# Performance work log

Hardware: AMD Instinct MI355X
Metric: run time of the kernel (lower is better)

The kernel has to match this reference:

```python
import jax, jax.numpy as jnp
import numpy as np

N, D, K = 16384, 256, 4096  # encoded vectors, embedding_dim, codebook_size


def setup_inputs() -> dict:
    key = jax.random.key(0)
    k_ze, k_cb = jax.random.split(key)
    ze = jax.random.normal(k_ze, (N, D), dtype=jnp.float32)
    codebook = jax.random.normal(k_cb, (K, D), dtype=jnp.float32)
    return {"ze": ze, "codebook": codebook}


def reference(ze, codebook):
    # Pairwise squared distances: ||ze||^2 + ||e||^2 - 2 ze e^T  -> [N, K]
    sq_norm = (
        jnp.sum(ze ** 2, axis=-1, keepdims=True)
        + jnp.sum(codebook ** 2, axis=1)
        - 2.0 * jnp.matmul(ze, codebook.T)
    )
    indices = jnp.argmin(sq_norm, axis=-1)            # [N]
    zq = jnp.take(codebook, indices, axis=0)          # [N, D] gather

    # VQ losses (stop-gradient mirrors .detach())
    vq_e_loss = jnp.mean((zq - jax.lax.stop_gradient(ze)) ** 2)
    vq_commit_loss = jnp.mean((jax.lax.stop_gradient(zq) - ze) ** 2)

    # perplexity: probs[i] = count_i / 10 (faithful to original, incl. /10)
    counts = jnp.zeros((K,), dtype=jnp.float32).at[indices].add(1.0)
    probs = counts / 10.0
    perplexity = jnp.exp(-jnp.sum(probs * jnp.log(probs + 1e-10)))

    return indices, zq, vq_e_loss, vq_commit_loss, perplexity
```

## Files before the change

### kernel.cpp

```cpp
#include <hip/hip_runtime.h>
#include <math.h>

#define N_TOT 16384
#define DIM   256
#define KCB   4096

typedef __attribute__((ext_vector_type(8)))  short s8v;
typedef __attribute__((ext_vector_type(16))) float f16v;

#define PK_OFF   32832
#define CBF_OFF  163904
#define WS_NEED  4358208ull
#define ZERO_W   36880

__device__ __forceinline__ void gload16(const void* g, void* l) {
  __builtin_amdgcn_global_load_lds(
      (const __attribute__((address_space(1))) unsigned int*)g,
      (__attribute__((address_space(3))) unsigned int*)l, 16, 0, 0);
}

__global__ __launch_bounds__(256)
void cb_prep_k(const float* __restrict__ cb, float* __restrict__ ws) {
  const int t = threadIdx.x, tile = blockIdx.x;
  for (int i = tile * 256 + t; i < ZERO_W; i += 128 * 256) ws[KCB + i] = 0.0f;

  const int col = t >> 3, j = t & 7;
  const int c0  = tile * 32;
  ushort* tb = (ushort*)((char*)ws + CBF_OFF) + (size_t)tile * 16384;
  const float* src = cb + (size_t)(c0 + col) * DIM;
  float s = 0.0f;
  #pragma unroll
  for (int ks = 0; ks < 16; ++ks) {
    #pragma unroll
    for (int kh = 0; kh < 2; ++kh) {
      float x = src[ks * 16 + kh * 8 + j];
      s += x * x;
      unsigned xb = __float_as_uint(x);
      unsigned hb = xb & 0xFFFF0000u;
      float lf = x - __uint_as_float(hb);
      tb[ks * 512 + kh * 256 + t]        = (ushort)(xb >> 16);
      tb[8192 + ks * 512 + kh * 256 + t] = (ushort)(__float_as_uint(lf) >> 16);
    }
  }
  s += __shfl_down(s, 4, 8);
  s += __shfl_down(s, 2, 8);
  s += __shfl_down(s, 1, 8);
  if (j == 0) ws[c0 + col] = s;
}

#define AP 260

__global__ __launch_bounds__(512, 2)
void vq_mfma_k(const float* __restrict__ ze, float* __restrict__ ws) {
  __shared__ __align__(16) char ldsU[66560];

  const int t    = threadIdx.x;
  const int lane = t & 63;
  const int w    = t >> 6;
  const int ln31 = lane & 31;
  const int hl   = lane >> 5;
  const int mb   = blockIdx.x >> 2;
  const int cq   = blockIdx.x & 3;
  const int m0   = mb * 256;

  const float* cbn = ws;
  unsigned long long* pk = (unsigned long long*)((char*)ws + PK_OFF);
  const char* cbF = (const char*)ws + CBF_OFF;

  s8v ah[16], al[16];
  float* Af = (float*)ldsU;
  for (int c = 0; c < 4; ++c) {
    __syncthreads();
    {
      int r  = t >> 3;
      int f0 = t & 7;
      const float* src = ze + (size_t)(m0 + c * 64 + r) * DIM;
      #pragma unroll
      for (int i = 0; i < 8; ++i) {
        int f = f0 + 8 * i;
        *(float4*)&Af[r * AP + f * 4] = *(const float4*)(src + f * 4);
      }
    }
    __syncthreads();
    if ((w >> 1) == c) {
      int rl = (w & 1) * 32 + ln31;
      #pragma unroll
      for (int ks = 0; ks < 16; ++ks) {
        float4 x0 = *(const float4*)&Af[rl * AP + ks * 16 + hl * 8];
        float4 x1 = *(const float4*)&Af[rl * AP + ks * 16 + hl * 8 + 4];
        float xs[8] = {x0.x, x0.y, x0.z, x0.w, x1.x, x1.y, x1.z, x1.w};
        #pragma unroll
        for (int j = 0; j < 8; ++j) {
          unsigned xb = __float_as_uint(xs[j]);
          unsigned hb = xb & 0xFFFF0000u;
          float lf = xs[j] - __uint_as_float(hb);
          ah[ks][j] = (short)(xb >> 16);
          al[ks][j] = (short)(__float_as_uint(lf) >> 16);
        }
      }
    }
  }
  __syncthreads();

  char* bufs0 = ldsU;
  char* bufs1 = ldsU + 32768;
  const char* qbase = cbF + (size_t)cq * 32 * 32768;

  {
    const char* g = qbase + (size_t)w * 4096 + (size_t)lane * 16;
    char* lp = bufs0 + w * 4096;
    #pragma unroll
    for (int ii = 0; ii < 4; ++ii) gload16(g + ii * 1024, lp + ii * 1024);
  }

  float best[16];
  int   bidx[16];
  #pragma unroll
  for (int r = 0; r < 16; ++r) { best[r] = -1e30f; bidx[r] = 0; }

  #pragma unroll 1
  for (int tt = 0; tt < 32; ++tt) {
    __syncthreads();
    if (tt + 1 < 32) {
      const char* g = qbase + (size_t)(tt + 1) * 32768 + (size_t)w * 4096 + (size_t)lane * 16;
      char* lp = ((tt + 1) & 1 ? bufs1 : bufs0) + w * 4096;
      #pragma unroll
      for (int ii = 0; ii < 4; ++ii) gload16(g + ii * 1024, lp + ii * 1024);
    }

    const int   c0      = cq * 1024 + tt * 32;
    const float half_cv = 0.5f * cbn[c0 + ln31];
    const char* bc      = (tt & 1) ? bufs1 : bufs0;

    f16v hh, xx;
    #pragma unroll
    for (int r = 0; r < 16; ++r) { hh[r] = 0.0f; xx[r] = 0.0f; }

    #pragma unroll
    for (int ks = 0; ks < 16; ++ks) {
      s8v bh = *(const s8v*)(bc + ks * 1024 + lane * 16);
      s8v bl = *(const s8v*)(bc + 16384 + ks * 1024 + lane * 16);
      hh = __builtin_amdgcn_mfma_f32_32x32x16_bf16(ah[ks], bh, hh, 0, 0, 0);
      xx = __builtin_amdgcn_mfma_f32_32x32x16_bf16(ah[ks], bl, xx, 0, 0, 0);
      xx = __builtin_amdgcn_mfma_f32_32x32x16_bf16(al[ks], bh, xx, 0, 0, 0);
    }

    #pragma unroll
    for (int r = 0; r < 16; ++r) {
      float s = hh[r] + xx[r] - half_cv;
      if (s > best[r]) { best[r] = s; bidx[r] = c0 + ln31; }
    }
  }

  #pragma unroll
  for (int r = 0; r < 16; ++r) {
    float s = best[r];
    int   c = bidx[r];
    #pragma unroll
    for (int mk = 1; mk < 32; mk <<= 1) {
      float os = __shfl_xor(s, mk, 64);
      int   oc = __shfl_xor(c, mk, 64);
      if (os > s || (os == s && oc < c)) { s = os; c = oc; }
    }
    if (ln31 == 0) {
      int row = m0 + w * 32 + (r & 3) + 8 * (r >> 2) + 4 * hl;
      unsigned u = __float_as_uint(s);
      unsigned enc = (u & 0x80000000u) ? ~u : (u | 0x80000000u);
      unsigned long long p = ((unsigned long long)enc << 32) | (unsigned)(KCB - 1 - c);
      atomicMax(&pk[row], p);
    }
  }
}

__global__ __launch_bounds__(256)
void gather_k(const float* __restrict__ ze, const float* __restrict__ cb,
              float* __restrict__ ws, float* __restrict__ out) {
  __shared__ int sIdx[64];
  const int t  = threadIdx.x;
  const int m0 = blockIdx.x * 64;
  float* counts   = ws + KCB;
  float* loss_sum = ws + 2 * KCB;
  const unsigned long long* pk = (const unsigned long long*)((const char*)ws + PK_OFF);

  if (t < 64) {
    unsigned long long p = pk[m0 + t];
    int col = KCB - 1 - (int)(unsigned)(p & 0xFFFFFFFFull);
    out[m0 + t] = (float)col;
    sIdx[t] = col;
    atomicAdd(&counts[col], 1.0f);
  }
  __syncthreads();

  float* out_zq = out + N_TOT;
  const int w = t >> 6, ln = t & 63;
  float lsum = 0.0f;
  #pragma unroll
  for (int p = 0; p < 16; ++p) {
    int r = w + 4 * p;
    float4 cvv = *(const float4*)(cb + (size_t)sIdx[r] * DIM + ln * 4);
    float4 zv  = *(const float4*)(ze + (size_t)(m0 + r) * DIM + ln * 4);
    *(float4*)(out_zq + (size_t)(m0 + r) * DIM + ln * 4) = cvv;
    float dx = cvv.x - zv.x, dy = cvv.y - zv.y, dz = cvv.z - zv.z, dw = cvv.w - zv.w;
    lsum += dx * dx + dy * dy + dz * dz + dw * dw;
  }
  #pragma unroll
  for (int off = 32; off > 0; off >>= 1) lsum += __shfl_down(lsum, off, 64);
  if (ln == 0) atomicAdd(loss_sum, lsum);
}

__global__ void zero_ws_k(float* __restrict__ ws, int nw) {
  int i = blockIdx.x * 256 + threadIdx.x;
  if (i < nw) ws[KCB + i] = 0.0f;
}

__global__ void cbnorm_k(const float* __restrict__ cb, float* __restrict__ ws) {
  int row  = blockIdx.x * 4 + (threadIdx.x >> 6);
  int lane = threadIdx.x & 63;
  float4 v = *(const float4*)(cb + (size_t)row * DIM + lane * 4);
  float s = v.x*v.x + v.y*v.y + v.z*v.z + v.w*v.w;
  #pragma unroll
  for (int off = 32; off > 0; off >>= 1) s += __shfl_down(s, off, 64);
  if (lane == 0) ws[row] = s;
}

#define FBM 32
#define FBN 64
#define FBD 128
__global__ __launch_bounds__(256, 4)
void vq_main_k(const float* __restrict__ ze, const float* __restrict__ cb,
               float* __restrict__ ws, float* __restrict__ out) {
  __shared__ float As[FBM * FBD];
  __shared__ float Bs[FBN * FBD];
  __shared__ float red_d[FBM * 16];
  __shared__ int   red_i[FBM * 16];
  __shared__ int   sIdx[FBM];

  const int t  = threadIdx.x;
  const int tx = t & 15;
  const int ty = t >> 4;
  const int m0 = blockIdx.x * FBM;

  const float* cbn = ws;
  float* counts    = ws + KCB;
  float* loss_sum  = ws + 2 * KCB;

  float best0 = 1e30f, best1 = 1e30f;
  int   bidx0 = 0,     bidx1 = 0;
  const int sA = ty & 7;
  const int sB = tx & 7;

  for (int kt = 0; kt < KCB / FBN; ++kt) {
    float cbnj[4];
    #pragma unroll
    for (int j = 0; j < 4; ++j) cbnj[j] = cbn[kt * FBN + tx + 16 * j];
    float acc[2][4];
    #pragma unroll
    for (int i = 0; i < 2; ++i)
      #pragma unroll
      for (int j = 0; j < 4; ++j) acc[i][j] = 0.0f;

    for (int dc = 0; dc < DIM / FBD; ++dc) {
      __syncthreads();
      {
        int c  = t & 31;
        int rb = t >> 5;
        #pragma unroll
        for (int p = 0; p < 4; ++p) {
          int r = rb + 8 * p;
          float4 v = *(const float4*)(ze + (size_t)(m0 + r) * DIM + dc * FBD + c * 4);
          *(float4*)&As[r * FBD + ((c ^ (r & 7)) << 2)] = v;
        }
        #pragma unroll
        for (int p = 0; p < 8; ++p) {
          int r = rb + 8 * p;
          float4 v = *(const float4*)(cb + (size_t)(kt * FBN + r) * DIM + dc * FBD + c * 4);
          *(float4*)&Bs[r * FBD + ((c ^ (r & 7)) << 2)] = v;
        }
      }
      __syncthreads();
      #pragma unroll 8
      for (int ds = 0; ds < FBD / 4; ++ds) {
        float4 a0 = *(const float4*)&As[ty * FBD + ((ds ^ sA) << 2)];
        float4 a1 = *(const float4*)&As[(ty + 16) * FBD + ((ds ^ sA) << 2)];
        float4 b[4];
        #pragma unroll
        for (int j = 0; j < 4; ++j)
          b[j] = *(const float4*)&Bs[(tx + 16 * j) * FBD + ((ds ^ sB) << 2)];
        #pragma unroll
        for (int j = 0; j < 4; ++j) {
          acc[0][j] = fmaf(a0.x, b[j].x, acc[0][j]);
          acc[0][j] = fmaf(a0.y, b[j].y, acc[0][j]);
          acc[0][j] = fmaf(a0.z, b[j].z, acc[0][j]);
          acc[0][j] = fmaf(a0.w, b[j].w, acc[0][j]);
          acc[1][j] = fmaf(a1.x, b[j].x, acc[1][j]);
          acc[1][j] = fmaf(a1.y, b[j].y, acc[1][j]);
          acc[1][j] = fmaf(a1.z, b[j].z, acc[1][j]);
          acc[1][j] = fmaf(a1.w, b[j].w, acc[1][j]);
        }
      }
    }
    #pragma unroll
    for (int j = 0; j < 4; ++j) {
      int kg = kt * FBN + tx + 16 * j;
      float d0 = cbnj[j] - 2.0f * acc[0][j];
      float d1 = cbnj[j] - 2.0f * acc[1][j];
      if (d0 < best0) { best0 = d0; bidx0 = kg; }
      if (d1 < best1) { best1 = d1; bidx1 = kg; }
    }
  }

  __syncthreads();
  red_d[ty * 16 + tx] = best0;        red_i[ty * 16 + tx] = bidx0;
  red_d[(ty + 16) * 16 + tx] = best1; red_i[(ty + 16) * 16 + tx] = bidx1;
  __syncthreads();

  if (t < FBM) {
    float bd = red_d[t * 16]; int bi = red_i[t * 16];
    #pragma unroll
    for (int q = 1; q < 16; ++q) {
      float d = red_d[t * 16 + q]; int i2 = red_i[t * 16 + q];
      if (d < bd || (d == bd && i2 < bi)) { bd = d; bi = i2; }
    }
    out[m0 + t] = (float)bi;
    sIdx[t] = bi;
    atomicAdd(&counts[bi], 1.0f);
  }
  __syncthreads();

  float* out_zq = out + N_TOT;
  const int wv = t >> 6, ln = t & 63;
  float lsum = 0.0f;
  #pragma unroll
  for (int p = 0; p < 8; ++p) {
    int r = wv + 4 * p;
    float4 cvv = *(const float4*)(cb + (size_t)sIdx[r] * DIM + ln * 4);
    float4 zv  = *(const float4*)(ze + (size_t)(m0 + r) * DIM + ln * 4);
    *(float4*)(out_zq + (size_t)(m0 + r) * DIM + ln * 4) = cvv;
    float dx = cvv.x - zv.x, dy = cvv.y - zv.y, dz = cvv.z - zv.z, dw = cvv.w - zv.w;
    lsum += dx*dx + dy*dy + dz*dz + dw*dw;
  }
  #pragma unroll
  for (int off = 32; off > 0; off >>= 1) lsum += __shfl_down(lsum, off, 64);
  if (ln == 0) atomicAdd(loss_sum, lsum);
}

__global__ void finalize_k(const float* __restrict__ ws, float* __restrict__ out) {
  __shared__ float red[256];
  int t = threadIdx.x;
  const float* counts = ws + KCB;
  float s = 0.0f;
  for (int k = t; k < KCB; k += 256) {
    float p = counts[k] * 0.1f;
    s += p * logf(p + 1e-10f);
  }
  red[t] = s;
  __syncthreads();
  for (int q = 128; q > 0; q >>= 1) { if (t < q) red[t] += red[t + q]; __syncthreads(); }
  if (t == 0) {
    float loss = ws[2 * KCB] / (float)((size_t)N_TOT * DIM);
    float* o = out + N_TOT + (size_t)N_TOT * DIM;
    o[0] = loss;
    o[1] = loss;
    o[2] = expf(-red[0]);
  }
}

extern "C" void kernel_launch(void* const* d_in, const int* in_sizes, int n_in,
                              void* d_out, int out_size, void* d_ws, size_t ws_size,
                              hipStream_t stream) {
  const float* ze = (const float*)d_in[0];
  const float* cb = (const float*)d_in[1];
  float* out = (float*)d_out;
  float* ws  = (float*)d_ws;

  if (ws_size >= WS_NEED) {
    cb_prep_k<<<128, 256, 0, stream>>>(cb, ws);
    vq_mfma_k<<<256, 512, 0, stream>>>(ze, ws);
    gather_k<<<N_TOT / 64, 256, 0, stream>>>(ze, cb, ws, out);
  } else {
    zero_ws_k<<<(KCB + 1 + 255) / 256, 256, 0, stream>>>(ws, KCB + 1);
    cbnorm_k<<<KCB / 4, 256, 0, stream>>>(cb, ws);
    vq_main_k<<<N_TOT / FBM, 256, 0, stream>>>(ze, cb, ws, out);
  }
  finalize_k<<<1, 256, 0, stream>>>(ws, out);
}
```

Before: 192.9 us.

## Triple-buffer codebook tiles with prefetch distance two and explicit vmcnt waits

```diff
diff --git a/kernel.cpp b/kernel.cpp
--- a/kernel.cpp
+++ b/kernel.cpp
@@ -52,7 +52,8 @@
 
 __global__ __launch_bounds__(512, 2)
 void vq_mfma_k(const float* __restrict__ ze, float* __restrict__ ws) {
-  __shared__ __align__(16) char ldsU[66560];
+  __shared__ __align__(16) char ldsU[3 * 32768 + 4096];
+  float* sCbn = (float*)(ldsU + 3 * 32768);
 
   const int t    = threadIdx.x;
   const int lane = t & 63;
@@ -100,15 +101,18 @@
       }
     }
   }
-  __syncthreads();
-
-  char* bufs0 = ldsU;
-  char* bufs1 = ldsU + 32768;
+  if (t < 512) {
+    sCbn[t]       = cbn[cq * 1024 + t];
+    sCbn[t + 512] = cbn[cq * 1024 + 512 + t];
+  }
+  __syncthreads();
+
   const char* qbase = cbF + (size_t)cq * 32 * 32768;
 
-  {
-    const char* g = qbase + (size_t)w * 4096 + (size_t)lane * 16;
-    char* lp = bufs0 + w * 4096;
+  #pragma unroll
+  for (int pt = 0; pt < 2; ++pt) {
+    const char* g = qbase + (size_t)pt * 32768 + (size_t)w * 4096 + (size_t)lane * 16;
+    char* lp = ldsU + pt * 32768 + w * 4096;
     #pragma unroll
     for (int ii = 0; ii < 4; ++ii) gload16(g + ii * 1024, lp + ii * 1024);
   }
@@ -118,24 +122,32 @@
   #pragma unroll
   for (int r = 0; r < 16; ++r) { best[r] = -1e30f; bidx[r] = 0; }
 
+  const char* bR = ldsU;
+  char*       bW = ldsU + 2 * 32768;
+
   #pragma unroll 1
   for (int tt = 0; tt < 32; ++tt) {
-    __syncthreads();
-    if (tt + 1 < 32) {
-      const char* g = qbase + (size_t)(tt + 1) * 32768 + (size_t)w * 4096 + (size_t)lane * 16;
-      char* lp = ((tt + 1) & 1 ? bufs1 : bufs0) + w * 4096;
+    if (tt == 31) { asm volatile("s_waitcnt vmcnt(0)" ::: "memory"); }
+    else          { asm volatile("s_waitcnt vmcnt(4)" ::: "memory"); }
+    __builtin_amdgcn_s_barrier();
+    __builtin_amdgcn_sched_barrier(0);
+
+    if (tt + 2 < 32) {
+      const char* g = qbase + (size_t)(tt + 2) * 32768 + (size_t)w * 4096 + (size_t)lane * 16;
+      char* lp = bW + w * 4096;
       #pragma unroll
       for (int ii = 0; ii < 4; ++ii) gload16(g + ii * 1024, lp + ii * 1024);
     }
 
     const int   c0      = cq * 1024 + tt * 32;
-    const float half_cv = 0.5f * cbn[c0 + ln31];
-    const char* bc      = (tt & 1) ? bufs1 : bufs0;
+    const float half_cv = 0.5f * sCbn[tt * 32 + ln31];
+    const char* bc      = bR;
 
     f16v hh, xx;
     #pragma unroll
     for (int r = 0; r < 16; ++r) { hh[r] = 0.0f; xx[r] = 0.0f; }
 
+    __builtin_amdgcn_s_setprio(1);
     #pragma unroll
     for (int ks = 0; ks < 16; ++ks) {
       s8v bh = *(const s8v*)(bc + ks * 1024 + lane * 16);
@@ -144,12 +156,16 @@
       xx = __builtin_amdgcn_mfma_f32_32x32x16_bf16(ah[ks], bl, xx, 0, 0, 0);
       xx = __builtin_amdgcn_mfma_f32_32x32x16_bf16(al[ks], bh, xx, 0, 0, 0);
     }
+    __builtin_amdgcn_s_setprio(0);
 
     #pragma unroll
     for (int r = 0; r < 16; ++r) {
       float s = hh[r] + xx[r] - half_cv;
       if (s > best[r]) { best[r] = s; bidx[r] = c0 + ln31; }
     }
+
+    bR += 32768; if (bR == ldsU + 3 * 32768) bR = ldsU;
+    bW += 32768; if (bW == ldsU + 3 * 32768) bW = ldsU;
   }
 
   #pragma unroll
```

After: 194.5 us. No clear change (+0.8%).

## Stream codebook tiles directly from global into registers instead of LDS staging

Applied to the files above, without the earlier changes.

```diff
diff --git a/kernel.cpp b/kernel.cpp
--- a/kernel.cpp
+++ b/kernel.cpp
@@ -12,12 +12,6 @@
 #define CBF_OFF  163904
 #define WS_NEED  4358208ull
 #define ZERO_W   36880
-
-__device__ __forceinline__ void gload16(const void* g, void* l) {
-  __builtin_amdgcn_global_load_lds(
-      (const __attribute__((address_space(1))) unsigned int*)g,
-      (__attribute__((address_space(3))) unsigned int*)l, 16, 0, 0);
-}
 
 __global__ __launch_bounds__(256)
 void cb_prep_k(const float* __restrict__ cb, float* __restrict__ ws) {
@@ -52,7 +46,8 @@
 
 __global__ __launch_bounds__(512, 2)
 void vq_mfma_k(const float* __restrict__ ze, float* __restrict__ ws) {
-  __shared__ __align__(16) char ldsU[66560];
+  __shared__ __align__(16) char ldsU[66560 + 4096];
+  float* sCbn = (float*)(ldsU + 66560);
 
   const int t    = threadIdx.x;
   const int lane = t & 63;
@@ -100,54 +95,52 @@
       }
     }
   }
-  __syncthreads();
-
-  char* bufs0 = ldsU;
-  char* bufs1 = ldsU + 32768;
-  const char* qbase = cbF + (size_t)cq * 32 * 32768;
-
-  {
-    const char* g = qbase + (size_t)w * 4096 + (size_t)lane * 16;
-    char* lp = bufs0 + w * 4096;
-    #pragma unroll
-    for (int ii = 0; ii < 4; ++ii) gload16(g + ii * 1024, lp + ii * 1024);
-  }
+  sCbn[t]       = cbn[cq * 1024 + t];
+  sCbn[t + 512] = cbn[cq * 1024 + 512 + t];
+  __syncthreads();
+
+  const char* qb = cbF + (size_t)cq * 32 * 32768 + (size_t)lane * 16;
 
   float best[16];
   int   bidx[16];
   #pragma unroll
   for (int r = 0; r < 16; ++r) { best[r] = -1e30f; bidx[r] = 0; }
 
+  s8v cbh = *(const s8v*)(qb);
+  s8v cbl = *(const s8v*)(qb + 16384);
+
   #pragma unroll 1
   for (int tt = 0; tt < 32; ++tt) {
-    __syncthreads();
-    if (tt + 1 < 32) {
-      const char* g = qbase + (size_t)(tt + 1) * 32768 + (size_t)w * 4096 + (size_t)lane * 16;
-      char* lp = ((tt + 1) & 1 ? bufs1 : bufs0) + w * 4096;
-      #pragma unroll
-      for (int ii = 0; ii < 4; ++ii) gload16(g + ii * 1024, lp + ii * 1024);
-    }
-
-    const int   c0      = cq * 1024 + tt * 32;
-    const float half_cv = 0.5f * cbn[c0 + ln31];
-    const char* bc      = (tt & 1) ? bufs1 : bufs0;
-
-    f16v hh, xx;
-    #pragma unroll
-    for (int r = 0; r < 16; ++r) { hh[r] = 0.0f; xx[r] = 0.0f; }
+    __builtin_amdgcn_s_barrier();
+    const char* tb = qb + (size_t)tt * 32768;
+    const float half_cv = 0.5f * sCbn[tt * 32 + ln31];
+
+    f16v acc;
+    #pragma unroll
+    for (int r = 0; r < 16; ++r) acc[r] = -half_cv;
 
     #pragma unroll
     for (int ks = 0; ks < 16; ++ks) {
-      s8v bh = *(const s8v*)(bc + ks * 1024 + lane * 16);
-      s8v bl = *(const s8v*)(bc + 16384 + ks * 1024 + lane * 16);
-      hh = __builtin_amdgcn_mfma_f32_32x32x16_bf16(ah[ks], bh, hh, 0, 0, 0);
-      xx = __builtin_amdgcn_mfma_f32_32x32x16_bf16(ah[ks], bl, xx, 0, 0, 0);
-      xx = __builtin_amdgcn_mfma_f32_32x32x16_bf16(al[ks], bh, xx, 0, 0, 0);
-    }
-
+      s8v nbh, nbl;
+      if (ks < 15) {
+        nbh = *(const s8v*)(tb + (ks + 1) * 1024);
+        nbl = *(const s8v*)(tb + 16384 + (ks + 1) * 1024);
+      } else if (tt < 31) {
+        nbh = *(const s8v*)(tb + 32768);
+        nbl = *(const s8v*)(tb + 32768 + 16384);
+      } else {
+        nbh = cbh; nbl = cbl;
+      }
+      acc = __builtin_amdgcn_mfma_f32_32x32x16_bf16(ah[ks], cbh, acc, 0, 0, 0);
+      acc = __builtin_amdgcn_mfma_f32_32x32x16_bf16(ah[ks], cbl, acc, 0, 0, 0);
+      acc = __builtin_amdgcn_mfma_f32_32x32x16_bf16(al[ks], cbh, acc, 0, 0, 0);
+      cbh = nbh; cbl = nbl;
+    }
+
+    const int c0 = cq * 1024 + tt * 32;
     #pragma unroll
     for (int r = 0; r < 16; ++r) {
-      float s = hh[r] + xx[r] - half_cv;
+      float s = acc[r];
       if (s > best[r]) { best[r] = s; bidx[r] = c0 + ln31; }
     }
   }
```

Result: slower. 215.3 us (+11.6%).
